# Optimization experiments

Measured on AMD Instinct MI355X. Metric: run time of the kernel, lower is better.

Reference implementation:

```python
import jax, jax.numpy as jnp
import numpy as np

ATTR_LEN = [2, 4, 4, 8]  # sums to 18 = MLP output dim; prod = 256 cases
USER_EMB_DIM = 256
B = 8192


def build_cases(attr_len):
    # Cartesian product of per-attribute one-hots -> [prod(attr_len), sum(attr_len)]
    out = np.eye(attr_len[0], dtype=np.float32)
    for n in attr_len[1:]:
        m = np.eye(n, dtype=np.float32)
        out = np.concatenate(
            [np.repeat(out, n, axis=0), np.tile(m, (out.shape[0], 1))], axis=1)
    return out


def setup_inputs() -> dict:
    key = jax.random.key(0)
    ks = jax.random.split(key, 8)
    d = USER_EMB_DIM
    x = jax.random.normal(ks[0], (B, d), dtype=jnp.float32)
    y = jax.random.uniform(ks[1], (B, 18), dtype=jnp.float32)
    # nn.Linear-style params (scaled normals)
    W1 = jax.random.normal(ks[2], (d, 50), dtype=jnp.float32) / np.sqrt(d)
    b1 = jnp.zeros((50,), dtype=jnp.float32)
    W2 = jax.random.normal(ks[3], (50, 32), dtype=jnp.float32) / np.sqrt(50.0)
    b2 = jnp.zeros((32,), dtype=jnp.float32)
    W3 = jax.random.normal(ks[4], (32, 18), dtype=jnp.float32) / np.sqrt(32.0)
    b3 = jnp.zeros((18,), dtype=jnp.float32)
    cases = jnp.asarray(build_cases(ATTR_LEN))  # [256, 18]
    return {"x": x, "y": y, "W1": W1, "b1": b1, "W2": W2, "b2": b2,
            "W3": W3, "b3": b3, "cases": cases}


def reference(x, y, W1, b1, W2, b2, W3, b3, cases):
    # MLP: user_emb_dim -> 50 -> 32 -> 18, sigmoid activations on hidden layers
    h = jax.nn.sigmoid(x @ W1 + b1)
    h = jax.nn.sigmoid(h @ W2 + b2)
    W_user = h @ W3 + b3                                  # [B, 18]
    # Partition function over all combinatorial label cases, fused into one
    # GEMM + logsumexp (original loops over cases with exp+accumulate).
    log_denom = jax.nn.logsumexp(W_user @ cases.T, axis=1)  # [B]
    # obj_i = exp(sum_j W_user[i].y[j]) / denom_i ; loss = -sum log obj
    S = jnp.sum(W_user @ y.T, axis=1)                     # [B] (via [B,B] mm, as original)
    loss = -jnp.sum(S - log_denom)
    # 'logit' in the original is W_user detached to numpy; return the array.
    return W_user, loss
```

## Files before the change

### kernel.cpp

```cpp
#include <hip/hip_runtime.h>

#define NB   8192
#define ND   256
#define NH1  50
#define NH2  32
#define NH3  18
#define RPB  16
#define NBLK (NB / RPB)
#define W1TS 260
#define WSS  40


__device__ __forceinline__ float sigmoidf_fast(float v) {
    return 1.0f / (1.0f + __expf(-v));
}

__global__ __launch_bounds__(256) void fused_main(
    const float* __restrict__ x, const float* __restrict__ y,
    const float* __restrict__ W1, const float* __restrict__ b1,
    const float* __restrict__ W2, const float* __restrict__ b2,
    const float* __restrict__ W3, const float* __restrict__ b3,
    float* __restrict__ out, float* __restrict__ ws)
{
    __shared__ float w1t[NH1 * W1TS];
    __shared__ float w2l[NH1 * NH2];
    __shared__ float w3l[NH2 * NH3];
    __shared__ float h2l[RPB][NH2 + 2];
    __shared__ float wul[RPB][NH3 + 1];

    const int t    = threadIdx.x;
    const int row  = t >> 4;
    const int ksl  = t & 15;
    const int grow = blockIdx.x * RPB + row;

    const float* xrow = x + (size_t)grow * ND + ksl * 4;
    const float4 xv0 = *reinterpret_cast<const float4*>(xrow + 0);
    const float4 xv1 = *reinterpret_cast<const float4*>(xrow + 64);
    const float4 xv2 = *reinterpret_cast<const float4*>(xrow + 128);
    const float4 xv3 = *reinterpret_cast<const float4*>(xrow + 192);

    for (int e = t; e < ND * NH1; e += 256) {
        int k = e / NH1;
        int j = e - k * NH1;
        w1t[j * W1TS + k] = W1[e];
    }
    for (int e = t; e < NH1 * NH2; e += 256) w2l[e] = W2[e];
    for (int e = t; e < NH2 * NH3; e += 256) w3l[e] = W3[e];
    __syncthreads();

    float h1[NH1];
#pragma unroll
    for (int j = 0; j < NH1; ++j) {
        const float* wj = &w1t[j * W1TS + ksl * 4];
        const float4 w0 = *reinterpret_cast<const float4*>(wj + 0);
        const float4 w1v = *reinterpret_cast<const float4*>(wj + 64);
        const float4 w2v = *reinterpret_cast<const float4*>(wj + 128);
        const float4 w3v = *reinterpret_cast<const float4*>(wj + 192);
        float a;
        a = xv0.x * w0.x;
        a = fmaf(xv0.y, w0.y, a);
        a = fmaf(xv0.z, w0.z, a);
        a = fmaf(xv0.w, w0.w, a);
        a = fmaf(xv1.x, w1v.x, a);
        a = fmaf(xv1.y, w1v.y, a);
        a = fmaf(xv1.z, w1v.z, a);
        a = fmaf(xv1.w, w1v.w, a);
        a = fmaf(xv2.x, w2v.x, a);
        a = fmaf(xv2.y, w2v.y, a);
        a = fmaf(xv2.z, w2v.z, a);
        a = fmaf(xv2.w, w2v.w, a);
        a = fmaf(xv3.x, w3v.x, a);
        a = fmaf(xv3.y, w3v.y, a);
        a = fmaf(xv3.z, w3v.z, a);
        a = fmaf(xv3.w, w3v.w, a);
        h1[j] = a;
    }
#pragma unroll
    for (int j = 0; j < NH1; ++j) {
        float v = h1[j];
        v += __shfl_xor(v, 1, 64);
        v += __shfl_xor(v, 2, 64);
        v += __shfl_xor(v, 4, 64);
        v += __shfl_xor(v, 8, 64);
        h1[j] = sigmoidf_fast(v + b1[j]);
    }

    {
        const float2 bb = *reinterpret_cast<const float2*>(b2 + 2 * ksl);
        float h2a = bb.x, h2b = bb.y;
#pragma unroll
        for (int j = 0; j < NH1; ++j) {
            const float2 w = *reinterpret_cast<const float2*>(&w2l[j * NH2 + 2 * ksl]);
            h2a = fmaf(h1[j], w.x, h2a);
            h2b = fmaf(h1[j], w.y, h2b);
        }
        h2a = sigmoidf_fast(h2a);
        h2b = sigmoidf_fast(h2b);
        *reinterpret_cast<float2*>(&h2l[row][2 * ksl]) = make_float2(h2a, h2b);
    }
    __syncthreads();

    {
        float a0 = b3[ksl];
        float a1 = (ksl < 2) ? b3[16 + ksl] : 0.0f;
#pragma unroll
        for (int j = 0; j < NH2; ++j) {
            const float h = h2l[row][j];
            a0 = fmaf(h, w3l[j * NH3 + ksl], a0);
            if (ksl < 2) a1 = fmaf(h, w3l[j * NH3 + 16 + ksl], a1);
        }
        wul[row][ksl] = a0;
        out[(size_t)grow * NH3 + ksl] = a0;
        if (ksl < 2) {
            wul[row][16 + ksl] = a1;
            out[(size_t)grow * NH3 + 16 + ksl] = a1;
        }
    }
    __syncthreads();

    if (t < 64) {
        const bool act = t < RPB;
        float wv[NH3], yv[NH3];
        float ld = 0.0f;
        if (act) {
            const float* yrow = y + (size_t)(blockIdx.x * RPB + t) * NH3;
#pragma unroll
            for (int c = 0; c < NH3; ++c) {
                wv[c] = wul[t][c];
                yv[c] = yrow[c];
            }
            float m = fmaxf(wv[0], wv[1]);
            ld += m + __logf(__expf(wv[0] - m) + __expf(wv[1] - m));
            m = fmaxf(fmaxf(wv[2], wv[3]), fmaxf(wv[4], wv[5]));
            ld += m + __logf(__expf(wv[2] - m) + __expf(wv[3] - m) +
                             __expf(wv[4] - m) + __expf(wv[5] - m));
            m = fmaxf(fmaxf(wv[6], wv[7]), fmaxf(wv[8], wv[9]));
            ld += m + __logf(__expf(wv[6] - m) + __expf(wv[7] - m) +
                             __expf(wv[8] - m) + __expf(wv[9] - m));
            m = wv[10];
#pragma unroll
            for (int i = 11; i < NH3; ++i) m = fmaxf(m, wv[i]);
            float s = 0.0f;
#pragma unroll
            for (int i = 10; i < NH3; ++i) s += __expf(wv[i] - m);
            ld += m + __logf(s);
        } else {
#pragma unroll
            for (int c = 0; c < NH3; ++c) { wv[c] = 0.0f; yv[c] = 0.0f; }
        }

        ld += __shfl_xor(ld, 1, 64);
        ld += __shfl_xor(ld, 2, 64);
        ld += __shfl_xor(ld, 4, 64);
        ld += __shfl_xor(ld, 8, 64);
#pragma unroll
        for (int c = 0; c < NH3; ++c) {
            float v = wv[c];
            v += __shfl_xor(v, 1, 64);
            v += __shfl_xor(v, 2, 64);
            v += __shfl_xor(v, 4, 64);
            v += __shfl_xor(v, 8, 64);
            wv[c] = v;
            float u = yv[c];
            u += __shfl_xor(u, 1, 64);
            u += __shfl_xor(u, 2, 64);
            u += __shfl_xor(u, 4, 64);
            u += __shfl_xor(u, 8, 64);
            yv[c] = u;
        }
        if (t == 0) {
            float* slot = ws + (size_t)blockIdx.x * WSS;
#pragma unroll
            for (int c = 0; c < NH3; ++c) {
                slot[c]       = yv[c];
                slot[NH3 + c] = wv[c];
            }
            slot[36] = ld;
        }
    }
}

__global__ __launch_bounds__(256) void finalize_loss(
    const float* __restrict__ ws, float* __restrict__ out)
{
    __shared__ double part[4][37];
    const int t = threadIdx.x;
    const int w = t >> 6, l = t & 63;
    if (l < 37) {
        double a = 0.0;
        for (int b = w * (NBLK / 4); b < (w + 1) * (NBLK / 4); ++b)
            a += (double)ws[(size_t)b * WSS + l];
        part[w][l] = a;
    }
    __syncthreads();
    if (t == 0) {
        double tot[37];
#pragma unroll
        for (int c = 0; c < 37; ++c)
            tot[c] = part[0][c] + part[1][c] + part[2][c] + part[3][c];
        double s = 0.0;
#pragma unroll
        for (int c = 0; c < NH3; ++c)
            s += tot[NH3 + c] * tot[c];
        out[(size_t)NB * NH3] = (float)(-(s - tot[36]));
    }
}

extern "C" void kernel_launch(void* const* d_in, const int* in_sizes, int n_in,
                              void* d_out, int out_size, void* d_ws, size_t ws_size,
                              hipStream_t stream) {
    const float* x  = (const float*)d_in[0];
    const float* y  = (const float*)d_in[1];
    const float* W1 = (const float*)d_in[2];
    const float* b1 = (const float*)d_in[3];
    const float* W2 = (const float*)d_in[4];
    const float* b2 = (const float*)d_in[5];
    const float* W3 = (const float*)d_in[6];
    const float* b3 = (const float*)d_in[7];
    float* out = (float*)d_out;
    float* ws  = (float*)d_ws;

    fused_main<<<dim3(NBLK), dim3(256), 0, stream>>>(x, y, W1, b1, W2, b2, W3, b3, out, ws);
    finalize_loss<<<dim3(1), dim3(256), 0, stream>>>(ws, out);
}
```

Before: 102.8 us.

## Stage W1 into LDS with direct global-to-LDS loads and DPP reductions

W1 is now copied into shared memory untransposed with 16-byte global_load_lds instructions. This replaces the scalar per-element transposing copy, which used an integer divide per element. The first-layer dot product is reorganised so each lane handles pairs of K indices and reads float2 weight pairs from the row-major layout. Cross-lane 16-wide sums now use DPP adds instead of ds_swizzle/shuffles, and one __syncthreads between the h2 write and read is removed because the same wave owns each row. The trade-off is possible LDS bank conflicts from the stride-50 row layout and a reliance on wave-lockstep ordering for the dropped barrier.

```diff
diff --git a/kernel.cpp b/kernel.cpp
--- a/kernel.cpp
+++ b/kernel.cpp
@@ -7,12 +7,30 @@
 #define NH3  18
 #define RPB  16
 #define NBLK (NB / RPB)
-#define W1TS 260
 #define WSS  40
 
 
 __device__ __forceinline__ float sigmoidf_fast(float v) {
     return 1.0f / (1.0f + __expf(-v));
+}
+
+template <int CTRL>
+__device__ __forceinline__ float dpp_addf(float v) {
+    return v + __int_as_float(__builtin_amdgcn_update_dpp(
+        0, __float_as_int(v), CTRL, 0xF, 0xF, true));
+}
+__device__ __forceinline__ float sum16(float v) {
+    v = dpp_addf<0xB1>(v);
+    v = dpp_addf<0x4E>(v);
+    v = dpp_addf<0x124>(v);
+    v = dpp_addf<0x128>(v);
+    return v;
+}
+
+__device__ __forceinline__ void gload_lds16(const float* g, float* l) {
+    __builtin_amdgcn_global_load_lds(
+        (const __attribute__((address_space(1))) unsigned int*)g,
+        (__attribute__((address_space(3))) unsigned int*)l, 16, 0, 0);
 }
 
 __global__ __launch_bounds__(256) void fused_main(
@@ -22,27 +40,30 @@
     const float* __restrict__ W3, const float* __restrict__ b3,
     float* __restrict__ out, float* __restrict__ ws)
 {
-    __shared__ float w1t[NH1 * W1TS];
-    __shared__ float w2l[NH1 * NH2];
-    __shared__ float w3l[NH2 * NH3];
-    __shared__ float h2l[RPB][NH2 + 2];
-    __shared__ float wul[RPB][NH3 + 1];
+    __shared__ alignas(16) float w1l[ND * NH1];
+    __shared__ alignas(16) float w2l[NH1 * NH2];
+    __shared__ alignas(16) float w3l[NH2 * NH3];
+    __shared__ alignas(16) float h2l[RPB][NH2 + 2];
+    __shared__ alignas(16) float wul[RPB][NH3 + 1];
 
     const int t    = threadIdx.x;
     const int row  = t >> 4;
     const int ksl  = t & 15;
+    const int lane = t & 63;
+    const int wave = t >> 6;
     const int grow = blockIdx.x * RPB + row;
 
-    const float* xrow = x + (size_t)grow * ND + ksl * 4;
-    const float4 xv0 = *reinterpret_cast<const float4*>(xrow + 0);
-    const float4 xv1 = *reinterpret_cast<const float4*>(xrow + 64);
-    const float4 xv2 = *reinterpret_cast<const float4*>(xrow + 128);
-    const float4 xv3 = *reinterpret_cast<const float4*>(xrow + 192);
-
-    for (int e = t; e < ND * NH1; e += 256) {
-        int k = e / NH1;
-        int j = e - k * NH1;
-        w1t[j * W1TS + k] = W1[e];
+    const float* xrow = x + (size_t)grow * ND + 2 * ksl;
+    float2 xv[8];
+#pragma unroll
+    for (int c = 0; c < 8; ++c)
+        xv[c] = *reinterpret_cast<const float2*>(xrow + 32 * c);
+
+#pragma unroll
+    for (int i = 0; i < 13; ++i) {
+        const int c = wave + 4 * i;
+        if (c < 50)
+            gload_lds16(W1 + c * 256 + lane * 4, w1l + c * 256);
     }
     for (int e = t; e < NH1 * NH2; e += 256) w2l[e] = W2[e];
     for (int e = t; e < NH2 * NH3; e += 256) w3l[e] = W3[e];
@@ -50,40 +71,24 @@
 
     float h1[NH1];
 #pragma unroll
-    for (int j = 0; j < NH1; ++j) {
-        const float* wj = &w1t[j * W1TS + ksl * 4];
-        const float4 w0 = *reinterpret_cast<const float4*>(wj + 0);
-        const float4 w1v = *reinterpret_cast<const float4*>(wj + 64);
-        const float4 w2v = *reinterpret_cast<const float4*>(wj + 128);
-        const float4 w3v = *reinterpret_cast<const float4*>(wj + 192);
-        float a;
-        a = xv0.x * w0.x;
-        a = fmaf(xv0.y, w0.y, a);
-        a = fmaf(xv0.z, w0.z, a);
-        a = fmaf(xv0.w, w0.w, a);
-        a = fmaf(xv1.x, w1v.x, a);
-        a = fmaf(xv1.y, w1v.y, a);
-        a = fmaf(xv1.z, w1v.z, a);
-        a = fmaf(xv1.w, w1v.w, a);
-        a = fmaf(xv2.x, w2v.x, a);
-        a = fmaf(xv2.y, w2v.y, a);
-        a = fmaf(xv2.z, w2v.z, a);
-        a = fmaf(xv2.w, w2v.w, a);
-        a = fmaf(xv3.x, w3v.x, a);
-        a = fmaf(xv3.y, w3v.y, a);
-        a = fmaf(xv3.z, w3v.z, a);
-        a = fmaf(xv3.w, w3v.w, a);
-        h1[j] = a;
-    }
-#pragma unroll
-    for (int j = 0; j < NH1; ++j) {
-        float v = h1[j];
-        v += __shfl_xor(v, 1, 64);
-        v += __shfl_xor(v, 2, 64);
-        v += __shfl_xor(v, 4, 64);
-        v += __shfl_xor(v, 8, 64);
-        h1[j] = sigmoidf_fast(v + b1[j]);
-    }
+    for (int j = 0; j < NH1; ++j) h1[j] = 0.0f;
+#pragma unroll
+    for (int c = 0; c < 8; ++c) {
+        const int kA = 32 * c + 2 * ksl;
+        const float* wA = &w1l[kA * NH1];
+        const float* wB = wA + NH1;
+        const float xa = xv[c].x, xb = xv[c].y;
+#pragma unroll
+        for (int jj = 0; jj < 25; ++jj) {
+            const float2 a = *reinterpret_cast<const float2*>(wA + 2 * jj);
+            const float2 b = *reinterpret_cast<const float2*>(wB + 2 * jj);
+            h1[2 * jj]     = fmaf(xa, a.x, fmaf(xb, b.x, h1[2 * jj]));
+            h1[2 * jj + 1] = fmaf(xa, a.y, fmaf(xb, b.y, h1[2 * jj + 1]));
+        }
+    }
+#pragma unroll
+    for (int j = 0; j < NH1; ++j)
+        h1[j] = sigmoidf_fast(sum16(h1[j]) + b1[j]);
 
     {
         const float2 bb = *reinterpret_cast<const float2*>(b2 + 2 * ksl);
@@ -98,7 +103,6 @@
         h2b = sigmoidf_fast(h2b);
         *reinterpret_cast<float2*>(&h2l[row][2 * ksl]) = make_float2(h2a, h2b);
     }
-    __syncthreads();
 
     {
         float a0 = b3[ksl];
@@ -149,24 +153,11 @@
             for (int c = 0; c < NH3; ++c) { wv[c] = 0.0f; yv[c] = 0.0f; }
         }
 
-        ld += __shfl_xor(ld, 1, 64);
-        ld += __shfl_xor(ld, 2, 64);
-        ld += __shfl_xor(ld, 4, 64);
-        ld += __shfl_xor(ld, 8, 64);
+        ld = sum16(ld);
 #pragma unroll
         for (int c = 0; c < NH3; ++c) {
-            float v = wv[c];
-            v += __shfl_xor(v, 1, 64);
-            v += __shfl_xor(v, 2, 64);
-            v += __shfl_xor(v, 4, 64);
-            v += __shfl_xor(v, 8, 64);
-            wv[c] = v;
-            float u = yv[c];
-            u += __shfl_xor(u, 1, 64);
-            u += __shfl_xor(u, 2, 64);
-            u += __shfl_xor(u, 4, 64);
-            u += __shfl_xor(u, 8, 64);
-            yv[c] = u;
+            wv[c] = sum16(wv[c]);
+            yv[c] = sum16(yv[c]);
         }
         if (t == 0) {
             float* slot = ws + (size_t)blockIdx.x * WSS;
```

New measurement: 94.73 us. 1.09x faster.
